# Kernel optimization log

Measured on AMD Instinct MI355X. Metric: run time of the kernel, lower is better.

Reference implementation:

```python
import jax, jax.numpy as jnp
import numpy as np

N = 100000      # nodes
E = 1600000     # message-passing edges
P = 1000000     # prediction edges
DIN = 128       # node_in_channels
H = 128         # hidden_channels
DOUT = 64       # out_channels (node embedding)
EIN = 32        # edge_in_channels
EPS = 1e-5


def setup_inputs() -> dict:
    key = jax.random.key(0)
    ks = iter(jax.random.split(key, 48))
    nk = lambda: next(ks)
    rn = lambda shape: jax.random.normal(nk(), shape, dtype=jnp.float32)
    glorot = lambda shape: rn(shape) * (1.0 / np.sqrt(shape[-1]))
    inp = {
        "x": rn((N, DIN)),
        "edge_index": jax.random.randint(nk(), (2, E), 0, N),
        "pred_edge_index": jax.random.randint(nk(), (2, P), 0, N),
        "edge_features": rn((P, EIN)),
        # SAGEConv layer 1: lin_l (aggregated, with bias), lin_r (root, no bias)
        "sage1_Wl": glorot((H, DIN)), "sage1_bl": jnp.zeros((H,), jnp.float32), "sage1_Wr": glorot((H, DIN)),
        "bn1_g": jnp.ones((H,), jnp.float32), "bn1_b": jnp.zeros((H,), jnp.float32),
        "bn1_m": rn((H,)) * 0.1, "bn1_v": jnp.ones((H,), jnp.float32),
        # SAGEConv layer 2
        "sage2_Wl": glorot((DOUT, H)), "sage2_bl": jnp.zeros((DOUT,), jnp.float32), "sage2_Wr": glorot((DOUT, H)),
        # edge MLP: Linear(EIN, H//2) -> BN -> ReLU -> Linear(H//2, H//4)
        "edge_W1": glorot((H // 2, EIN)), "edge_b1": jnp.zeros((H // 2,), jnp.float32),
        "ebn_g": jnp.ones((H // 2,), jnp.float32), "ebn_b": jnp.zeros((H // 2,), jnp.float32),
        "ebn_m": rn((H // 2,)) * 0.1, "ebn_v": jnp.ones((H // 2,), jnp.float32),
        "edge_W2": glorot((H // 4, H // 2)), "edge_b2": jnp.zeros((H // 4,), jnp.float32),
        # predictor: Linear(2*DOUT+H//4, H) -> BN -> ReLU -> Linear(H, H//2) -> BN -> ReLU -> Linear(H//2, 1)
        "p_W1": glorot((H, 2 * DOUT + H // 4)), "p_b1": jnp.zeros((H,), jnp.float32),
        "pbn1_g": jnp.ones((H,), jnp.float32), "pbn1_b": jnp.zeros((H,), jnp.float32),
        "pbn1_m": rn((H,)) * 0.1, "pbn1_v": jnp.ones((H,), jnp.float32),
        "p_W2": glorot((H // 2, H)), "p_b2": jnp.zeros((H // 2,), jnp.float32),
        "pbn2_g": jnp.ones((H // 2,), jnp.float32), "pbn2_b": jnp.zeros((H // 2,), jnp.float32),
        "pbn2_m": rn((H // 2,)) * 0.1, "pbn2_v": jnp.ones((H // 2,), jnp.float32),
        "p_W3": glorot((1, H // 2)), "p_b3": jnp.zeros((1,), jnp.float32),
    }
    return inp


def _bn(h, g, b, m, v):
    # eval-mode BatchNorm1d with running stats
    return (h - m) * (g / jnp.sqrt(v + EPS)) + b


def _sage(h, src, dst, Wl, bl, Wr):
    # PyG SAGEConv (mean aggr): lin_l(mean of h[src] at dst) + lin_r(h)
    msg = jax.ops.segment_sum(h[src], dst, num_segments=N)        # [N, d]
    cnt = jax.ops.segment_sum(jnp.ones((src.shape[0],), h.dtype), dst, num_segments=N)
    agg = msg / jnp.maximum(cnt, 1.0)[:, None]
    return agg @ Wl.T + bl + h @ Wr.T


def reference(x, edge_index, pred_edge_index, edge_features,
              sage1_Wl, sage1_bl, sage1_Wr, bn1_g, bn1_b, bn1_m, bn1_v,
              sage2_Wl, sage2_bl, sage2_Wr,
              edge_W1, edge_b1, ebn_g, ebn_b, ebn_m, ebn_v, edge_W2, edge_b2,
              p_W1, p_b1, pbn1_g, pbn1_b, pbn1_m, pbn1_v,
              p_W2, p_b2, pbn2_g, pbn2_b, pbn2_m, pbn2_v, p_W3, p_b3):
    src, dst = edge_index[0], edge_index[1]
    # GraphSAGE encoder (eval mode: dropout off, BN running stats)
    h = _sage(x, src, dst, sage1_Wl, sage1_bl, sage1_Wr)
    h = jax.nn.relu(_bn(h, bn1_g, bn1_b, bn1_m, bn1_v))
    z = _sage(h, src, dst, sage2_Wl, sage2_bl, sage2_Wr)          # [N, DOUT]
    # edge-pair gather + concat
    combined = jnp.concatenate([z[pred_edge_index[0]], z[pred_edge_index[1]]], axis=-1)  # [P, 2*DOUT]
    # edge feature MLP
    e = edge_features @ edge_W1.T + edge_b1
    e = jax.nn.relu(_bn(e, ebn_g, ebn_b, ebn_m, ebn_v))
    e = e @ edge_W2.T + edge_b2                                   # [P, H//4]
    combined = jnp.concatenate([combined, e], axis=-1)            # [P, 2*DOUT + H//4]
    # predictor MLP
    u = combined @ p_W1.T + p_b1
    u = jax.nn.relu(_bn(u, pbn1_g, pbn1_b, pbn1_m, pbn1_v))
    u = u @ p_W2.T + p_b2
    u = jax.nn.relu(_bn(u, pbn2_g, pbn2_b, pbn2_m, pbn2_v))
    out = u @ p_W3.T + p_b3                                       # [P, 1]
    return out[:, 0]
```

## Files before the change

kernel.cpp:

```cpp
#include <hip/hip_runtime.h>

#define Nn 100000
#define Ee 1600000
#define Pp 1000000
#define EPSf 1e-5f

typedef _Float16 f16x8 __attribute__((ext_vector_type(8)));
typedef _Float16 f16x4 __attribute__((ext_vector_type(4)));
typedef _Float16 f16x2 __attribute__((ext_vector_type(2)));
typedef float f32x4 __attribute__((ext_vector_type(4)));

__device__ __forceinline__ float4 ld4(const float* p) { return *(const float4*)p; }

#define oW1l 0
#define oW1r 16384
#define oW2l 32768
#define oW2r 40960
#define oW1a 49152
#define oW1b 57344
#define oW1c 65536
#define oWe1 69632
#define oWe2 71680
#define oWp2 73728
#define W16_TOTAL 81920

#define BN_TOTAL 608

#define NBUC 391
#define SCAP 1024
#define SGROUPS 8

__global__ __launch_bounds__(256) void prep_kernel(
    const float* __restrict__ x,
    const float* __restrict__ s1Wl, const float* __restrict__ s1Wr,
    const float* __restrict__ s2Wl, const float* __restrict__ s2Wr,
    const float* __restrict__ pW1,  const float* __restrict__ eW1,
    const float* __restrict__ eW2,  const float* __restrict__ pW2,
    const float* __restrict__ eb1,
    const float* __restrict__ ebng, const float* __restrict__ ebnb,
    const float* __restrict__ ebnm, const float* __restrict__ ebnv,
    const float* __restrict__ eb2,
    const float* __restrict__ pb1,
    const float* __restrict__ p1g, const float* __restrict__ p1b,
    const float* __restrict__ p1m, const float* __restrict__ p1v,
    const float* __restrict__ pb2,
    const float* __restrict__ p2g, const float* __restrict__ p2b,
    const float* __restrict__ p2m, const float* __restrict__ p2v,
    const float* __restrict__ pW3,
    _Float16* __restrict__ w16, float* __restrict__ bnA,
    _Float16* __restrict__ x16) {
    int tid = blockIdx.x * 256 + threadIdx.x;
    if (tid < W16_TOTAL) {
        float v;
        if (tid < 16384)      v = s1Wl[tid];
        else if (tid < 32768) v = s1Wr[tid - 16384];
        else if (tid < 40960) v = s2Wl[tid - 32768];
        else if (tid < 49152) v = s2Wr[tid - 40960];
        else if (tid < 57344) { int l = tid - 49152; v = pW1[(l >> 6) * 160 + (l & 63)]; }
        else if (tid < 65536) { int l = tid - 57344; v = pW1[(l >> 6) * 160 + 64 + (l & 63)]; }
        else if (tid < 69632) { int l = tid - 65536; v = pW1[(l >> 5) * 160 + 128 + (l & 31)]; }
        else if (tid < 71680) v = eW1[tid - 69632];
        else if (tid < 73728) v = eW2[tid - 71680];
        else                  v = pW2[tid - 73728];
        w16[tid] = (_Float16)v;
    } else if (tid < W16_TOTAL + BN_TOTAL) {
        int b = tid - W16_TOTAL;
        float v;
        if (b < 64)       v = ebng[b] * rsqrtf(ebnv[b] + EPSf);
        else if (b < 128) { int c = b - 64;  float s = ebng[c] * rsqrtf(ebnv[c] + EPSf);
                            v = (eb1[c] - ebnm[c]) * s + ebnb[c]; }
        else if (b < 256) { int c = b - 128; v = p1g[c] * rsqrtf(p1v[c] + EPSf); }
        else if (b < 384) { int c = b - 256; float s = p1g[c] * rsqrtf(p1v[c] + EPSf);
                            v = (pb1[c] - p1m[c]) * s + p1b[c]; }
        else if (b < 448) { int c = b - 384; v = p2g[c] * rsqrtf(p2v[c] + EPSf); }
        else if (b < 512) { int c = b - 448; float s = p2g[c] * rsqrtf(p2v[c] + EPSf);
                            v = (pb2[c] - p2m[c]) * s + p2b[c]; }
        else if (b < 544) v = eb2[b - 512];
        else              v = pW3[b - 544];
        bnA[b] = v;
    }
    int stride = gridDim.x * 256;
    const int NV = Nn * 128 / 4;
    for (int i = tid; i < NV; i += stride) {
        float4 v = ((const float4*)x)[i];
        f16x4 h = {(_Float16)v.x, (_Float16)v.y, (_Float16)v.z, (_Float16)v.w};
        ((f16x4*)x16)[i] = h;
    }
}

__global__ __launch_bounds__(256) void bucket_kernel(
    const int* __restrict__ src, const int* __restrict__ dst,
    unsigned* __restrict__ deg,
    unsigned* __restrict__ stage, unsigned* __restrict__ gcur) {
    const int g = blockIdx.x & 7;
    const unsigned gb = g * NBUC;
    int stride = gridDim.x * 256;
    for (int i = blockIdx.x * 256 + threadIdx.x; i < Ee; i += stride) {
        int d = dst[i];
        int s = src[i];
        atomicAdd(&deg[d], 1u);
        int b = d >> 8;
        unsigned p = atomicAdd(&gcur[gb + b], 1u);
        stage[((size_t)(gb + b)) * SCAP + p] = ((unsigned)s << 8) | (unsigned)(d & 255);
    }
}

__global__ __launch_bounds__(1024) void scanA_kernel(const unsigned* __restrict__ deg,
                                                     unsigned* __restrict__ escan,
                                                     unsigned* __restrict__ bsum) {
    __shared__ unsigned s[1024];
    int t = threadIdx.x;
    int gid = blockIdx.x * 1024 + t;
    unsigned v = (gid < Nn) ? deg[gid] : 0u;
    s[t] = v;
    __syncthreads();
    for (int off = 1; off < 1024; off <<= 1) {
        unsigned u = (t >= off) ? s[t - off] : 0u;
        __syncthreads();
        s[t] += u;
        __syncthreads();
    }
    if (gid < Nn) escan[gid] = s[t] - v;
    if (t == 1023) bsum[blockIdx.x] = s[1023];
}

__global__ __launch_bounds__(128) void scanB_kernel(const unsigned* __restrict__ bsum,
                                                    unsigned* __restrict__ boff,
                                                    int nblk) {
    __shared__ unsigned s[128];
    int t = threadIdx.x;
    unsigned v = (t < nblk) ? bsum[t] : 0u;
    s[t] = v;
    __syncthreads();
    for (int off = 1; off < 128; off <<= 1) {
        unsigned u = (t >= off) ? s[t - off] : 0u;
        __syncthreads();
        s[t] += u;
        __syncthreads();
    }
    if (t < nblk) boff[t] = s[t] - v;
}

__global__ __launch_bounds__(1024) void scanC_kernel(const unsigned* __restrict__ escan,
                                                     const unsigned* __restrict__ boff,
                                                     int* __restrict__ rowptr) {
    int t = threadIdx.x;
    int gid = blockIdx.x * 1024 + t;
    if (gid < Nn) rowptr[gid] = (int)(escan[gid] + boff[blockIdx.x]);
    if (gid == 0) rowptr[Nn] = Ee;
}

__global__ __launch_bounds__(256) void partC_kernel(
    const unsigned* __restrict__ stage, const unsigned* __restrict__ gcur,
    const int* __restrict__ rowptr, int* __restrict__ elist) {
    __shared__ int lbase[256];
    __shared__ unsigned lcur[256];
    const int b = blockIdx.x;
    const int n0 = b << 8;
    {
        int node = n0 + threadIdx.x;
        lbase[threadIdx.x] = (node < Nn) ? rowptr[node] : 0;
        lcur[threadIdx.x] = 0u;
    }
    __syncthreads();
#pragma unroll 1
    for (int g = 0; g < SGROUPS; ++g) {
        unsigned cnt = gcur[g * NBUC + b];
        const unsigned* sp = stage + ((size_t)(g * NBUC + b)) * SCAP;
        for (unsigned i = threadIdx.x; i < cnt; i += 256) {
            unsigned v = sp[i];
            int lidx = v & 255;
            int s = (int)(v >> 8);
            unsigned p = atomicAdd(&lcur[lidx], 1u);
            elist[lbase[lidx] + p] = s;
        }
    }
}

template<int W>
__global__ __launch_bounds__(256, 8) void aggregate16_kernel(
    const _Float16* __restrict__ feat,
    const int* __restrict__ rowptr,
    const int* __restrict__ elist,
    _Float16* __restrict__ outp) {
    int node = (blockIdx.x * 256 + threadIdx.x) >> 6;
    int lane = threadIdx.x & 63;
    if (node >= Nn) return;
    constexpr int SEGS = W / 8;
    constexpr int RPI  = 64 / SEGS;
    const int r = lane / SEGS, c = lane % SEGS;
    int beg = rowptr[node], end = rowptr[node + 1];
    int n = end - beg;
    float acc[8];
#pragma unroll
    for (int k = 0; k < 8; ++k) acc[k] = 0.f;
    for (int c0 = 0; c0 < n; c0 += 64) {
        int m = min(64, n - c0);
        int se = (lane < m) ? elist[beg + c0 + lane] : 0;
        int iters = (m + RPI - 1) / RPI;
#pragma unroll 2
        for (int i = 0; i < iters; ++i) {
            int j = i * RPI + r;
            int s = __shfl(se, j);
            if (j < m) {
                f16x8 v = *(const f16x8*)(feat + (size_t)s * W + c * 8);
#pragma unroll
                for (int k = 0; k < 8; ++k) acc[k] += (float)v[k];
            }
        }
    }
#pragma unroll
    for (int k = 0; k < 8; ++k) {
#pragma unroll
        for (int off = SEGS; off < 64; off <<= 1)
            acc[k] += __shfl_xor(acc[k], off);
    }
    if (r == 0) {
        float inv = 1.0f / fmaxf((float)n, 1.0f);
        f16x8 o;
#pragma unroll
        for (int k = 0; k < 8; ++k) o[k] = (_Float16)(acc[k] * inv);
        *(f16x8*)(outp + (size_t)node * W + c * 8) = o;
    }
}

__global__ __launch_bounds__(256) void dense1_kernel(
    const _Float16* __restrict__ A1, const _Float16* __restrict__ A2,
    const _Float16* __restrict__ W1, const _Float16* __restrict__ W2,
    const float* __restrict__ lb,
    const float* __restrict__ bng, const float* __restrict__ bnb,
    const float* __restrict__ bnm, const float* __restrict__ bnv,
    _Float16* __restrict__ out) {
    const int t = threadIdx.x;
    const int w = t >> 6, lane = t & 63;
    const int lrow = lane & 15, lq = lane >> 4;
    const int row0 = blockIdx.x * 64 + w * 16;
    const int ld = min(row0 + lrow, Nn - 1);

    f16x8 a1[4], a2[4];
#pragma unroll
    for (int i = 0; i < 4; ++i) {
        a1[i] = *(const f16x8*)(A1 + (size_t)ld * 128 + i * 32 + lq * 8);
        a2[i] = *(const f16x8*)(A2 + (size_t)ld * 128 + i * 32 + lq * 8);
    }
#pragma unroll
    for (int nt = 0; nt < 8; ++nt) {
        const _Float16* w1r = W1 + (size_t)(nt * 16 + lrow) * 128;
        const _Float16* w2r = W2 + (size_t)(nt * 16 + lrow) * 128;
        f32x4 c = {0.f, 0.f, 0.f, 0.f};
#pragma unroll
        for (int i = 0; i < 4; ++i) {
            c = __builtin_amdgcn_mfma_f32_16x16x32_f16(a1[i], *(const f16x8*)(w1r + i * 32 + lq * 8), c, 0, 0, 0);
            c = __builtin_amdgcn_mfma_f32_16x16x32_f16(a2[i], *(const f16x8*)(w2r + i * 32 + lq * 8), c, 0, 0, 0);
        }
        int cc = nt * 16 + lrow;
        float s = bng[cc] * rsqrtf(bnv[cc] + EPSf);
        float h = (lb[cc] - bnm[cc]) * s + bnb[cc];
#pragma unroll
        for (int r = 0; r < 4; ++r) {
            int gr = row0 + lq * 4 + r;
            if (gr < Nn)
                out[(size_t)gr * 128 + cc] = (_Float16)fmaxf(c[r] * s + h, 0.f);
        }
    }
}

__global__ __launch_bounds__(256) void gemmY_kernel(
    const _Float16* __restrict__ A, const _Float16* __restrict__ W,
    _Float16* __restrict__ out) {
    const int t = threadIdx.x;
    const int w = t >> 6, lane = t & 63;
    const int lrow = lane & 15, lq = lane >> 4;
    const int row0 = blockIdx.x * 64 + w * 16;
    const int ld = min(row0 + lrow, Nn - 1);
    f16x8 a[4];
#pragma unroll
    for (int i = 0; i < 4; ++i)
        a[i] = *(const f16x8*)(A + (size_t)ld * 128 + i * 32 + lq * 8);
#pragma unroll
    for (int nt = 0; nt < 4; ++nt) {
        const _Float16* wr = W + (size_t)(nt * 16 + lrow) * 128;
        f32x4 c = {0.f, 0.f, 0.f, 0.f};
#pragma unroll
        for (int i = 0; i < 4; ++i)
            c = __builtin_amdgcn_mfma_f32_16x16x32_f16(a[i], *(const f16x8*)(wr + i * 32 + lq * 8), c, 0, 0, 0);
        int cc = nt * 16 + lrow;
#pragma unroll
        for (int r = 0; r < 4; ++r) {
            int gr = row0 + lq * 4 + r;
            if (gr < Nn) out[(size_t)gr * 64 + cc] = (_Float16)c[r];
        }
    }
}

__global__ __launch_bounds__(256) void dense2b_kernel(
    const _Float16* __restrict__ aggY, const _Float16* __restrict__ A2,
    const _Float16* __restrict__ W2, const float* __restrict__ lb,
    _Float16* __restrict__ out) {
    const int t = threadIdx.x;
    const int w = t >> 6, lane = t & 63;
    const int lrow = lane & 15, lq = lane >> 4;
    const int row0 = blockIdx.x * 64 + w * 16;
    const int ld = min(row0 + lrow, Nn - 1);
    f16x8 a[4];
#pragma unroll
    for (int i = 0; i < 4; ++i)
        a[i] = *(const f16x8*)(A2 + (size_t)ld * 128 + i * 32 + lq * 8);
#pragma unroll
    for (int nt = 0; nt < 4; ++nt) {
        const _Float16* wr = W2 + (size_t)(nt * 16 + lrow) * 128;
        f32x4 c = {0.f, 0.f, 0.f, 0.f};
#pragma unroll
        for (int i = 0; i < 4; ++i)
            c = __builtin_amdgcn_mfma_f32_16x16x32_f16(a[i], *(const f16x8*)(wr + i * 32 + lq * 8), c, 0, 0, 0);
        int cc = nt * 16 + lrow;
        float b = lb[cc];
#pragma unroll
        for (int r = 0; r < 4; ++r) {
            int gr = row0 + lq * 4 + r;
            if (gr < Nn) {
                float g = (float)aggY[(size_t)gr * 64 + cc];
                out[(size_t)gr * 64 + cc] = (_Float16)(c[r] + g + b);
            }
        }
    }
}

__global__ __launch_bounds__(256) void emlp_kernel(
    const float* __restrict__ ef,
    const _Float16* __restrict__ w16,
    const float* __restrict__ bnA,
    _Float16* __restrict__ e2out) {
    __shared__ __align__(16) _Float16 E1[64 * 72];
    const int t = threadIdx.x;
    const int lane = t & 63, w = t >> 6;
    const int lrow = lane & 15, lq = lane >> 4;
    const int e0 = blockIdx.x * 64 + w * 16;
    const int erow = w * 16 + lrow;

    const float* src = ef + (size_t)(e0 + lrow) * 32 + lq * 8;
    float4 f0 = ld4(src), f1 = ld4(src + 4);
    f16x8 bf = {(_Float16)f0.x, (_Float16)f0.y, (_Float16)f0.z, (_Float16)f0.w,
                (_Float16)f1.x, (_Float16)f1.y, (_Float16)f1.z, (_Float16)f1.w};

#pragma unroll
    for (int nt = 0; nt < 4; ++nt) {
        f16x8 wf = *(const f16x8*)(w16 + oWe1 + (nt * 16 + lrow) * 32 + lq * 8);
        f32x4 c = {0.f, 0.f, 0.f, 0.f};
        c = __builtin_amdgcn_mfma_f32_16x16x32_f16(wf, bf, c, 0, 0, 0);
        int cb = nt * 16 + lq * 4;
        float4 s = *(const float4*)(bnA + cb);
        float4 h = *(const float4*)(bnA + 64 + cb);
        f16x4 o;
        o[0] = (_Float16)fmaxf(c[0] * s.x + h.x, 0.f);
        o[1] = (_Float16)fmaxf(c[1] * s.y + h.y, 0.f);
        o[2] = (_Float16)fmaxf(c[2] * s.z + h.z, 0.f);
        o[3] = (_Float16)fmaxf(c[3] * s.w + h.w, 0.f);
        *(f16x4*)(E1 + erow * 72 + cb) = o;
    }
    f16x8 a0 = *(const f16x8*)(E1 + erow * 72 + lq * 8);
    f16x8 a1 = *(const f16x8*)(E1 + erow * 72 + 32 + lq * 8);
#pragma unroll
    for (int nt = 0; nt < 2; ++nt) {
        f16x8 b0 = *(const f16x8*)(w16 + oWe2 + (nt * 16 + lrow) * 64 + lq * 8);
        f16x8 b1 = *(const f16x8*)(w16 + oWe2 + (nt * 16 + lrow) * 64 + 32 + lq * 8);
        f32x4 c = {0.f, 0.f, 0.f, 0.f};
        c = __builtin_amdgcn_mfma_f32_16x16x32_f16(b0, a0, c, 0, 0, 0);
        c = __builtin_amdgcn_mfma_f32_16x16x32_f16(b1, a1, c, 0, 0, 0);
        int cb = nt * 16 + lq * 4;
        float4 bias = *(const float4*)(bnA + 512 + cb);
        f16x4 o;
        o[0] = (_Float16)(c[0] + bias.x);
        o[1] = (_Float16)(c[1] + bias.y);
        o[2] = (_Float16)(c[2] + bias.z);
        o[3] = (_Float16)(c[3] + bias.w);
        *(f16x4*)(e2out + (size_t)(e0 + lrow) * 32 + cb) = o;
    }
}

#define EPB 256
#define NT  ((Pp + EPB - 1) / EPB)
#define EGRID 256

#define oL_W1a 0
#define oL_W1b 18432
#define oL_W1c 36864
#define oL_Wp2 47104
#define oL_BN  64512
#define oL_ZU  66304
#define SMEM_BYTES 135936

__global__ __launch_bounds__(1024, 4) void edge_kernel(
    const int* __restrict__ pe,
    const _Float16* __restrict__ e2,
    const _Float16* __restrict__ z,
    const _Float16* __restrict__ w16,
    const float* __restrict__ bnA,
    const float* __restrict__ pb3,
    float* __restrict__ out) {
    __shared__ __align__(16) unsigned char smem[SMEM_BYTES];
    _Float16* LW1a = (_Float16*)(smem + oL_W1a);
    _Float16* LW1b = (_Float16*)(smem + oL_W1b);
    _Float16* LW1c = (_Float16*)(smem + oL_W1c);
    _Float16* LWp2 = (_Float16*)(smem + oL_Wp2);
    float*    LBN  = (float*)(smem + oL_BN);
    _Float16* ZU   = (_Float16*)(smem + oL_ZU);

    const float* bn2s = LBN;        const float* bn2h = LBN + 128;
    const float* bn3s = LBN + 256;  const float* bn3h = LBN + 320;
    const float* wp3g = LBN + 384;

    const int t = threadIdx.x;
    const int lane = t & 63;
    const int w = t >> 6;
    const int m0 = w * 16;
    const int lrow = lane & 15;
    const int lq = lane >> 4;
    const float pb3v = pb3[0];

    auto load_idx = [&](int tl, int& ia, int& ib) {
        int e = min(tl * EPB + m0 + lrow, Pp - 1);
        ia = pe[e];
        ib = pe[Pp + e];
    };
    auto gather = [&](int tl, int ia, int ib, f16x8* F) {
        F[0] = *(const f16x8*)(z + (size_t)ia * 64 + lq * 8);
        F[1] = *(const f16x8*)(z + (size_t)ia * 64 + 32 + lq * 8);
        F[2] = *(const f16x8*)(z + (size_t)ib * 64 + lq * 8);
        F[3] = *(const f16x8*)(z + (size_t)ib * 64 + 32 + lq * 8);
        int e = min(tl * EPB + m0 + lrow, Pp - 1);
        F[4] = *(const f16x8*)(e2 + (size_t)e * 32 + lq * 8);
    };

    int tile = blockIdx.x;
    int ia1, ib1;
    {
        int ia0, ib0;
        load_idx(tile, ia0, ib0);
        load_idx(tile + EGRID, ia1, ib1);
        f16x8 F[5];
        gather(tile, ia0, ib0, F);

        { int r = t >> 3, s = t & 7;
          *(f16x8*)(LW1a + r * 72 + s * 8) = *(const f16x8*)(w16 + oW1a + r * 64 + s * 8);
          *(f16x8*)(LW1b + r * 72 + s * 8) = *(const f16x8*)(w16 + oW1b + r * 64 + s * 8); }
        if (t < 512) { int r = t >> 2, s = t & 3;
          *(f16x8*)(LW1c + r * 40 + s * 8) = *(const f16x8*)(w16 + oW1c + r * 32 + s * 8); }
        { int r = t >> 4, s = t & 15;
          *(f16x8*)(LWp2 + r * 136 + s * 8) = *(const f16x8*)(w16 + oWp2 + r * 128 + s * 8); }
        if (t < 384) LBN[t] = bnA[128 + t];
        else if (t < 448) LBN[t] = bnA[544 + (t - 384)];
        __syncthreads();

        const int erow = m0 + lrow;
        const int zr = erow * 136;
        for (; tile < NT; tile += EGRID) {
            f16x8 G[5];
            gather(tile + EGRID, ia1, ib1, G);
            int ia2, ib2;
            load_idx(tile + 2 * EGRID, ia2, ib2);

            const bool act = (tile * EPB + m0) < Pp;
            if (act) {
                __builtin_amdgcn_s_setprio(1);
#pragma unroll
                for (int nt = 0; nt < 8; ++nt) {
                    const _Float16* wa = LW1a + (nt * 16 + lrow) * 72;
                    const _Float16* wb = LW1b + (nt * 16 + lrow) * 72;
                    const _Float16* wc = LW1c + (nt * 16 + lrow) * 40;
                    f32x4 c = {0.f, 0.f, 0.f, 0.f};
                    c = __builtin_amdgcn_mfma_f32_16x16x32_f16(*(const f16x8*)(wa + lq * 8),      F[0], c, 0, 0, 0);
                    c = __builtin_amdgcn_mfma_f32_16x16x32_f16(*(const f16x8*)(wa + 32 + lq * 8), F[1], c, 0, 0, 0);
                    c = __builtin_amdgcn_mfma_f32_16x16x32_f16(*(const f16x8*)(wb + lq * 8),      F[2], c, 0, 0, 0);
                    c = __builtin_amdgcn_mfma_f32_16x16x32_f16(*(const f16x8*)(wb + 32 + lq * 8), F[3], c, 0, 0, 0);
                    c = __builtin_amdgcn_mfma_f32_16x16x32_f16(*(const f16x8*)(wc + lq * 8),      F[4], c, 0, 0, 0);
                    int cb = nt * 16 + lq * 4;
                    float4 s = *(const float4*)(bn2s + cb);
                    float4 h = *(const float4*)(bn2h + cb);
                    f16x4 o;
                    o[0] = (_Float16)fmaxf(c[0] * s.x + h.x, 0.f);
                    o[1] = (_Float16)fmaxf(c[1] * s.y + h.y, 0.f);
                    o[2] = (_Float16)fmaxf(c[2] * s.z + h.z, 0.f);
                    o[3] = (_Float16)fmaxf(c[3] * s.w + h.w, 0.f);
                    *(f16x4*)(ZU + zr + cb) = o;
                }
                __builtin_amdgcn_s_setprio(0);
                {
                    f16x8 a0 = *(const f16x8*)(ZU + zr + 0  + lq * 8);
                    f16x8 a1 = *(const f16x8*)(ZU + zr + 32 + lq * 8);
                    f16x8 a2 = *(const f16x8*)(ZU + zr + 64 + lq * 8);
                    f16x8 a3 = *(const f16x8*)(ZU + zr + 96 + lq * 8);
                    float acc = 0.f;
                    __builtin_amdgcn_s_setprio(1);
#pragma unroll
                    for (int nt = 0; nt < 4; ++nt) {
                        const _Float16* wr = LWp2 + (nt * 16 + lrow) * 136 + lq * 8;
                        f32x4 c = {0.f, 0.f, 0.f, 0.f};
                        c = __builtin_amdgcn_mfma_f32_16x16x32_f16(*(const f16x8*)(wr + 0),  a0, c, 0, 0, 0);
                        c = __builtin_amdgcn_mfma_f32_16x16x32_f16(*(const f16x8*)(wr + 32), a1, c, 0, 0, 0);
                        c = __builtin_amdgcn_mfma_f32_16x16x32_f16(*(const f16x8*)(wr + 64), a2, c, 0, 0, 0);
                        c = __builtin_amdgcn_mfma_f32_16x16x32_f16(*(const f16x8*)(wr + 96), a3, c, 0, 0, 0);
                        int cb = nt * 16 + lq * 4;
                        float4 s  = *(const float4*)(bn3s + cb);
                        float4 h  = *(const float4*)(bn3h + cb);
                        float4 w3 = *(const float4*)(wp3g + cb);
                        acc += fmaxf(c[0] * s.x + h.x, 0.f) * w3.x;
                        acc += fmaxf(c[1] * s.y + h.y, 0.f) * w3.y;
                        acc += fmaxf(c[2] * s.z + h.z, 0.f) * w3.z;
                        acc += fmaxf(c[3] * s.w + h.w, 0.f) * w3.w;
                    }
                    __builtin_amdgcn_s_setprio(0);
                    acc += __shfl_xor(acc, 16);
                    acc += __shfl_xor(acc, 32);
                    if (lane < 16) out[tile * EPB + m0 + lane] = acc + pb3v;
                }
            }
#pragma unroll
            for (int i = 0; i < 5; ++i) F[i] = G[i];
            ia1 = ia2; ib1 = ib2;
        }
    }
}

extern "C" void kernel_launch(void* const* d_in, const int* in_sizes, int n_in,
                              void* d_out, int out_size, void* d_ws, size_t ws_size,
                              hipStream_t stream) {
    const float* x    = (const float*)d_in[0];
    const int*   eidx = (const int*)d_in[1];
    const int*   pe   = (const int*)d_in[2];
    const float* ef   = (const float*)d_in[3];
    const float* s1Wl = (const float*)d_in[4];
    const float* s1bl = (const float*)d_in[5];
    const float* s1Wr = (const float*)d_in[6];
    const float* bn1g = (const float*)d_in[7];
    const float* bn1b = (const float*)d_in[8];
    const float* bn1m = (const float*)d_in[9];
    const float* bn1v = (const float*)d_in[10];
    const float* s2Wl = (const float*)d_in[11];
    const float* s2bl = (const float*)d_in[12];
    const float* s2Wr = (const float*)d_in[13];
    const float* eW1  = (const float*)d_in[14];
    const float* eb1  = (const float*)d_in[15];
    const float* ebng = (const float*)d_in[16];
    const float* ebnb = (const float*)d_in[17];
    const float* ebnm = (const float*)d_in[18];
    const float* ebnv = (const float*)d_in[19];
    const float* eW2  = (const float*)d_in[20];
    const float* eb2  = (const float*)d_in[21];
    const float* pW1  = (const float*)d_in[22];
    const float* pb1  = (const float*)d_in[23];
    const float* p1g  = (const float*)d_in[24];
    const float* p1b  = (const float*)d_in[25];
    const float* p1m  = (const float*)d_in[26];
    const float* p1v  = (const float*)d_in[27];
    const float* pW2  = (const float*)d_in[28];
    const float* pb2  = (const float*)d_in[29];
    const float* p2g  = (const float*)d_in[30];
    const float* p2b  = (const float*)d_in[31];
    const float* p2m  = (const float*)d_in[32];
    const float* p2v  = (const float*)d_in[33];
    const float* pW3  = (const float*)d_in[34];
    const float* pb3  = (const float*)d_in[35];
    float* out = (float*)d_out;

    char* wk = (char*)d_ws;
    auto carve = [&](size_t bytes) {
        char* p = wk;
        wk += (bytes + 255) & ~(size_t)255;
        return p;
    };
    unsigned*  deg    = (unsigned*)carve((size_t)Nn * 4);
    unsigned*  gcur   = (unsigned*)carve((size_t)SGROUPS * NBUC * 4);
    int*       rowptr = (int*)carve((size_t)(Nn + 1) * 4);
    int*       elist  = (int*)carve((size_t)Ee * 4);
    unsigned*  escan  = (unsigned*)carve((size_t)Nn * 4);
    unsigned*  bsum   = (unsigned*)carve(128 * 4);
    unsigned*  boff   = (unsigned*)carve(128 * 4);
    _Float16*  w16    = (_Float16*)carve((size_t)W16_TOTAL * 2);
    float*     bnA    = (float*)carve((size_t)BN_TOTAL * 4);
    _Float16*  bufX   = (_Float16*)carve((size_t)Nn * 128 * 2);
    _Float16*  bufA   = (_Float16*)carve((size_t)Nn * 128 * 2);
    _Float16*  bufH   = (_Float16*)carve((size_t)Nn * 128 * 2);
    _Float16*  e2buf  = (_Float16*)carve((size_t)Pp * 32 * 2);
    _Float16*  bufY   = bufX;
    _Float16*  bufZ   = bufX + (size_t)Nn * 64;
    _Float16*  bufAy  = bufA;
    unsigned*  stage  = (unsigned*)bufH;

    const int* e_src = eidx;
    const int* e_dst = eidx + Ee;
    const int SBLK = (Nn + 1023) / 1024;

    size_t degBytes = ((size_t)Nn * 4 + 255) & ~(size_t)255;
    hipMemsetAsync(deg, 0, degBytes + (size_t)SGROUPS * NBUC * 4, stream);

    prep_kernel<<<800, 256, 0, stream>>>(x, s1Wl, s1Wr, s2Wl, s2Wr, pW1, eW1, eW2, pW2,
                                         eb1, ebng, ebnb, ebnm, ebnv, eb2,
                                         pb1, p1g, p1b, p1m, p1v,
                                         pb2, p2g, p2b, p2m, p2v, pW3,
                                         w16, bnA, bufX);
    emlp_kernel<<<Pp / 64, 256, 0, stream>>>(ef, w16, bnA, e2buf);

    bucket_kernel<<<512, 256, 0, stream>>>(e_src, e_dst, deg, stage, gcur);
    scanA_kernel<<<SBLK, 1024, 0, stream>>>(deg, escan, bsum);
    scanB_kernel<<<1, 128, 0, stream>>>(bsum, boff, SBLK);
    scanC_kernel<<<SBLK, 1024, 0, stream>>>(escan, boff, rowptr);
    partC_kernel<<<NBUC, 256, 0, stream>>>(stage, gcur, rowptr, elist);

    aggregate16_kernel<128><<<Nn / 4, 256, 0, stream>>>(bufX, rowptr, elist, bufA);
    dense1_kernel<<<(Nn + 63) / 64, 256, 0, stream>>>(
        bufA, bufX, w16 + oW1l, w16 + oW1r, s1bl, bn1g, bn1b, bn1m, bn1v, bufH);

    gemmY_kernel<<<(Nn + 63) / 64, 256, 0, stream>>>(bufH, w16 + oW2l, bufY);
    aggregate16_kernel<64><<<Nn / 4, 256, 0, stream>>>(bufY, rowptr, elist, bufAy);
    dense2b_kernel<<<(Nn + 63) / 64, 256, 0, stream>>>(
        bufAy, bufH, w16 + oW2r, s2bl, bufZ);

    edge_kernel<<<EGRID, 1024, 0, stream>>>(pe, e2buf, bufZ, w16, bnA, pb3, out);
}
```

Baseline: 784.2 us.

## Build CSR with block-local histograms and LDS degree counting

Each block now histograms a 4096-edge chunk into 512-node destination buckets in shared memory. It reserves space with one global atomic per bucket, then writes its staged edges. Per-node degrees come from a separate kernel that counts each bucket in shared memory, which replaces the per-edge global atomicAdd on deg and the heavily contended bucket-cursor atomics. This adds a kernel launch and relies on each bucket's edge count fitting the fixed capacity of 9216.

```diff
diff --git a/kernel.cpp b/kernel.cpp
--- a/kernel.cpp
+++ b/kernel.cpp
@@ -26,9 +26,11 @@
 
 #define BN_TOTAL 608
 
-#define NBUC 391
-#define SCAP 1024
-#define SGROUPS 8
+#define BSH 9
+#define NB2 196
+#define SCAP2 9216
+#define ECHUNK 4096
+#define NCHUNK ((Ee + ECHUNK - 1) / ECHUNK)
 
 __global__ __launch_bounds__(256) void prep_kernel(
     const float* __restrict__ x,
@@ -88,21 +90,60 @@
     }
 }
 
-__global__ __launch_bounds__(256) void bucket_kernel(
+__global__ __launch_bounds__(256) void bucketA_kernel(
     const int* __restrict__ src, const int* __restrict__ dst,
-    unsigned* __restrict__ deg,
     unsigned* __restrict__ stage, unsigned* __restrict__ gcur) {
-    const int g = blockIdx.x & 7;
-    const unsigned gb = g * NBUC;
-    int stride = gridDim.x * 256;
-    for (int i = blockIdx.x * 256 + threadIdx.x; i < Ee; i += stride) {
-        int d = dst[i];
-        int s = src[i];
-        atomicAdd(&deg[d], 1u);
-        int b = d >> 8;
-        unsigned p = atomicAdd(&gcur[gb + b], 1u);
-        stage[((size_t)(gb + b)) * SCAP + p] = ((unsigned)s << 8) | (unsigned)(d & 255);
-    }
+    __shared__ unsigned hist[NB2];
+    __shared__ unsigned base[NB2];
+    const int t = threadIdx.x;
+    const int e0 = blockIdx.x * ECHUNK;
+    for (int u = t; u < NB2; u += 256) hist[u] = 0u;
+    __syncthreads();
+
+    int sv[16], dv[16];
+#pragma unroll
+    for (int k = 0; k < 16; ++k) {
+        int e = e0 + k * 256 + t;
+        if (e < Ee) {
+            sv[k] = src[e];
+            dv[k] = dst[e];
+            atomicAdd(&hist[dv[k] >> BSH], 1u);
+        } else dv[k] = -1;
+    }
+    __syncthreads();
+    for (int u = t; u < NB2; u += 256) {
+        unsigned h = hist[u];
+        base[u] = h ? atomicAdd(&gcur[u], h) : 0u;
+        hist[u] = 0u;
+    }
+    __syncthreads();
+#pragma unroll
+    for (int k = 0; k < 16; ++k) {
+        if (dv[k] >= 0) {
+            int b = dv[k] >> BSH;
+            unsigned p = atomicAdd(&hist[b], 1u);
+            stage[(size_t)b * SCAP2 + base[b] + p] =
+                ((unsigned)sv[k] << BSH) | (unsigned)(dv[k] & 511);
+        }
+    }
+}
+
+__global__ __launch_bounds__(256) void countC_kernel(
+    const unsigned* __restrict__ stage, const unsigned* __restrict__ gcur,
+    unsigned* __restrict__ deg) {
+    __shared__ unsigned cnt[512];
+    const int b = blockIdx.x;
+    const int t = threadIdx.x;
+    cnt[t] = 0u; cnt[t + 256] = 0u;
+    __syncthreads();
+    unsigned m = gcur[b];
+    const unsigned* sp = stage + (size_t)b * SCAP2;
+    for (unsigned i = t; i < m; i += 256)
+        atomicAdd(&cnt[sp[i] & 511], 1u);
+    __syncthreads();
+    int n0 = b << BSH;
+    if (n0 + t < Nn)       deg[n0 + t] = cnt[t];
+    if (n0 + 256 + t < Nn) deg[n0 + 256 + t] = cnt[t + 256];
 }
 
 __global__ __launch_bounds__(1024) void scanA_kernel(const unsigned* __restrict__ deg,
@@ -150,30 +191,25 @@
     if (gid == 0) rowptr[Nn] = Ee;
 }
 
-__global__ __launch_bounds__(256) void partC_kernel(
+__global__ __launch_bounds__(256) void scatterE_kernel(
     const unsigned* __restrict__ stage, const unsigned* __restrict__ gcur,
     const int* __restrict__ rowptr, int* __restrict__ elist) {
-    __shared__ int lbase[256];
-    __shared__ unsigned lcur[256];
+    __shared__ int lbase[512];
+    __shared__ unsigned cur[512];
     const int b = blockIdx.x;
-    const int n0 = b << 8;
-    {
-        int node = n0 + threadIdx.x;
-        lbase[threadIdx.x] = (node < Nn) ? rowptr[node] : 0;
-        lcur[threadIdx.x] = 0u;
-    }
-    __syncthreads();
-#pragma unroll 1
-    for (int g = 0; g < SGROUPS; ++g) {
-        unsigned cnt = gcur[g * NBUC + b];
-        const unsigned* sp = stage + ((size_t)(g * NBUC + b)) * SCAP;
-        for (unsigned i = threadIdx.x; i < cnt; i += 256) {
-            unsigned v = sp[i];
-            int lidx = v & 255;
-            int s = (int)(v >> 8);
-            unsigned p = atomicAdd(&lcur[lidx], 1u);
-            elist[lbase[lidx] + p] = s;
-        }
+    const int t = threadIdx.x;
+    const int n0 = b << BSH;
+    lbase[t]       = (n0 + t < Nn)       ? rowptr[n0 + t]       : 0;
+    lbase[t + 256] = (n0 + 256 + t < Nn) ? rowptr[n0 + 256 + t] : 0;
+    cur[t] = 0u; cur[t + 256] = 0u;
+    __syncthreads();
+    unsigned m = gcur[b];
+    const unsigned* sp = stage + (size_t)b * SCAP2;
+    for (unsigned i = t; i < m; i += 256) {
+        unsigned v = sp[i];
+        int lid = v & 511;
+        unsigned p = atomicAdd(&cur[lid], 1u);
+        elist[lbase[lid] + p] = (int)(v >> BSH);
     }
 }
 
@@ -570,7 +606,7 @@
         return p;
     };
     unsigned*  deg    = (unsigned*)carve((size_t)Nn * 4);
-    unsigned*  gcur   = (unsigned*)carve((size_t)SGROUPS * NBUC * 4);
+    unsigned*  gcur   = (unsigned*)carve((size_t)256 * 4);
     int*       rowptr = (int*)carve((size_t)(Nn + 1) * 4);
     int*       elist  = (int*)carve((size_t)Ee * 4);
     unsigned*  escan  = (unsigned*)carve((size_t)Nn * 4);
@@ -591,8 +627,7 @@
     const int* e_dst = eidx + Ee;
     const int SBLK = (Nn + 1023) / 1024;
 
-    size_t degBytes = ((size_t)Nn * 4 + 255) & ~(size_t)255;
-    hipMemsetAsync(deg, 0, degBytes + (size_t)SGROUPS * NBUC * 4, stream);
+    hipMemsetAsync(gcur, 0, 256 * 4, stream);
 
     prep_kernel<<<800, 256, 0, stream>>>(x, s1Wl, s1Wr, s2Wl, s2Wr, pW1, eW1, eW2, pW2,
                                          eb1, ebng, ebnb, ebnm, ebnv, eb2,
@@ -601,11 +636,12 @@
                                          w16, bnA, bufX);
     emlp_kernel<<<Pp / 64, 256, 0, stream>>>(ef, w16, bnA, e2buf);
 
-    bucket_kernel<<<512, 256, 0, stream>>>(e_src, e_dst, deg, stage, gcur);
+    bucketA_kernel<<<NCHUNK, 256, 0, stream>>>(e_src, e_dst, stage, gcur);
+    countC_kernel<<<NB2, 256, 0, stream>>>(stage, gcur, deg);
     scanA_kernel<<<SBLK, 1024, 0, stream>>>(deg, escan, bsum);
     scanB_kernel<<<1, 128, 0, stream>>>(bsum, boff, SBLK);
     scanC_kernel<<<SBLK, 1024, 0, stream>>>(escan, boff, rowptr);
-    partC_kernel<<<NBUC, 256, 0, stream>>>(stage, gcur, rowptr, elist);
+    scatterE_kernel<<<NB2, 256, 0, stream>>>(stage, gcur, rowptr, elist);
 
     aggregate16_kernel<128><<<Nn / 4, 256, 0, stream>>>(bufX, rowptr, elist, bufA);
     dense1_kernel<<<(Nn + 63) / 64, 256, 0, stream>>>(
```

Result: faster. 676.6 us (-13.7%).
